# Kernel tuning notes

Hardware: AMD Instinct MI355X
Metric: run time of the kernel (lower is better)

The kernel has to match this reference:

```python
import jax, jax.numpy as jnp
import numpy as np

B, C, N = 16, 256, 1024
D_QK, D_V, BINS = 64, 256, 32
EPS = 1e-5


def setup_inputs() -> dict:
    key = jax.random.key(0)
    ks = jax.random.split(key, 12)

    def xavier(k, shape):
        fan_in, fan_out = shape[1], shape[0]
        lim = (6.0 / (fan_in + fan_out)) ** 0.5
        return jax.random.uniform(k, shape, jnp.float32, -lim, lim)

    return {
        "x": jax.random.normal(ks[0], (B, C, N), jnp.float32),
        "discrete": jax.random.randint(ks[1], (B, N, 3), 0, BINS),
        "xyz": jax.random.uniform(ks[2], (B, N, 3), jnp.float32),
        "q_w": xavier(ks[3], (D_QK, C)),
        "k_w": xavier(ks[4], (D_QK, C)),
        "v_w": xavier(ks[5], (D_V, C)),
        "v_b": jnp.zeros((D_V,), jnp.float32),
        "trans_w": xavier(ks[6], (C, D_V)),
        "trans_b": jnp.zeros((C,), jnp.float32),
        "bn_gamma": jnp.ones((C,), jnp.float32),
        "bn_beta": jnp.zeros((C,), jnp.float32),
        "x_lt": xavier(ks[7], (2 * BINS - 1, D_QK)),
        "y_lt": xavier(ks[8], (2 * BINS - 1, D_QK)),
        "z_lt": xavier(ks[9], (2 * BINS - 1, D_QK)),
    }


def reference(x, discrete, xyz, q_w, k_w, v_w, v_b, trans_w, trans_b,
              bn_gamma, bn_beta, x_lt, y_lt, z_lt):
    # x: [B,C,N], discrete: [B,N,3] int bin coords in [0,BINS)
    n = x.shape[2]
    x_q = jnp.einsum('dc,bcn->bnd', q_w, x)                      # [B,N,d_qk]
    x_k = jnp.einsum('dc,bcn->bdn', k_w, x)                      # [B,d_qk,N]
    x_v = jnp.einsum('dc,bcn->bdn', v_w, x) + v_b[None, :, None]  # [B,d_v,N]

    energy = jnp.einsum('bnd,bdm->bnm', x_q, x_k)                # [B,N,N]

    def rel_term(lt, d):
        # q @ lookup-table then gather along relative bin index (irregular access)
        ql = jnp.einsum('bnd,rd->bnr', x_q, lt)                  # [B,N,2*BINS-1]
        idx = d[:, None, :] - d[:, :, None] + (BINS - 1)          # [B,N,N]
        return jnp.take_along_axis(ql, idx, axis=2)

    dx, dy, dz = discrete[..., 0], discrete[..., 1], discrete[..., 2]
    energy = energy + rel_term(x_lt, dx) + rel_term(y_lt, dy) + rel_term(z_lt, dz)

    energy = energy / (float(n) ** 0.5)                           # scale == 'root'
    attention = jax.nn.softmax(energy, axis=-1)

    x_r = jnp.einsum('bdn,bnm->bdm', x_v, attention)              # [B,d_v,N]

    # offset=True: trans_conv(x - x_r) -> BN (batch stats) -> ReLU -> residual
    h = x - x_r
    t = jnp.einsum('cd,bdn->bcn', trans_w, h) + trans_b[None, :, None]
    mean = t.mean(axis=(0, 2), keepdims=True)
    var = t.var(axis=(0, 2), keepdims=True)
    t = (t - mean) * jax.lax.rsqrt(var + EPS)
    t = t * bn_gamma[None, :, None] + bn_beta[None, :, None]
    x_r = jax.nn.relu(t)
    return x + x_r
```

## Files before the change

### kernel.cpp

```cpp
#include <hip/hip_runtime.h>
#include <math.h>

#define BB 16
#define CC 256
#define NN 1024
#define DQK_ 64
#define DV_ 256
#define NR 192
#define EPS_F 1e-5f

#define OFF_XT  ((size_t)0)
#define OFF_QB  ((size_t)2097152)
#define OFF_KB  ((size_t)2621440)
#define OFF_QL  ((size_t)3145728)
#define OFF_HT  ((size_t)2097152)
#define OFF_VB  ((size_t)6291456)
#define OFF_ATT ((size_t)8388608)
#define OFF_T   ((size_t)8388608)
#define OFF_WQK ((size_t)16777216)
#define OFF_WV  ((size_t)16793600)
#define OFF_WT  ((size_t)16826368)
#define OFF_LTB ((size_t)16859136)
#define OFF_BNS ((size_t)16865280)
#define OFF_BNQ ((size_t)16865536)

typedef __attribute__((ext_vector_type(8))) short short8;
typedef __attribute__((ext_vector_type(4))) float f32x4;

__device__ __forceinline__ unsigned short f2b(float f) {
    unsigned int u = __float_as_uint(f);
    u = u + 0x7fffu + ((u >> 16) & 1u);
    return (unsigned short)(u >> 16);
}
__device__ __forceinline__ float b2f(unsigned short s) {
    return __uint_as_float(((unsigned int)s) << 16);
}

__global__ __launch_bounds__(256) void k_prep(
    const float* __restrict__ qw, const float* __restrict__ kw,
    const float* __restrict__ vw, const float* __restrict__ tw,
    const float* __restrict__ xlt, const float* __restrict__ ylt,
    const float* __restrict__ zlt,
    unsigned short* __restrict__ Wqk, unsigned short* __restrict__ Wv,
    unsigned short* __restrict__ Wt, unsigned short* __restrict__ LTb,
    float* __restrict__ bnS, float* __restrict__ bnQ)
{
    if (blockIdx.x == 160) {
        bnS[threadIdx.x] = 0.f;
        bnQ[threadIdx.x] = 0.f;
        return;
    }
    if (blockIdx.x > 160) {
        const int o2 = (blockIdx.x - 161) * 256 + threadIdx.x;
        const int e = o2 * 4;
        const int r = e >> 6, d = e & 63;
        const int a = r >> 6, q = r & 63;
        ushort4 u;
        if (q < 63) {
            const float* lt = (a == 0) ? xlt : ((a == 1) ? ylt : zlt);
            const float4 v = *(const float4*)(lt + q * 64 + d);
            u.x = f2b(v.x); u.y = f2b(v.y); u.z = f2b(v.z); u.w = f2b(v.w);
        } else {
            u.x = u.y = u.z = u.w = 0;
        }
        *(ushort4*)(LTb + e) = u;
        return;
    }
    const int o = blockIdx.x * 256 + threadIdx.x;
    const float* src; unsigned short* dst;
    if (o < 8192) {
        const int e = o * 4;
        src = (e < 16384) ? (qw + e) : (kw + e - 16384);
        dst = Wqk + e;
    } else if (o < 24576) {
        const int e = (o - 8192) * 4;
        src = vw + e; dst = Wv + e;
    } else {
        const int e = (o - 24576) * 4;
        src = tw + e; dst = Wt + e;
    }
    const float4 v = *(const float4*)src;
    ushort4 u;
    u.x = f2b(v.x); u.y = f2b(v.y); u.z = f2b(v.z); u.w = f2b(v.w);
    *(ushort4*)dst = u;
}

__global__ __launch_bounds__(256) void k_xt(
    const float* __restrict__ x, unsigned short* __restrict__ xT)
{
    __shared__ float tile[64][68];
    const int b = blockIdx.z;
    const int c0 = blockIdx.y * 64;
    const int n0 = blockIdx.x * 64;
    const int tid = threadIdx.x;
    #pragma unroll
    for (int it = 0; it < 4; ++it) {
        const int r = it * 16 + (tid >> 4);
        const int c4 = (tid & 15) * 4;
        *(float4*)&tile[r][c4] =
            *(const float4*)(x + ((size_t)b * CC + c0 + r) * NN + n0 + c4);
    }
    __syncthreads();
    const int n = tid >> 2;
    const int cg2 = (tid & 3) * 16;
    alignas(16) unsigned short buf[16];
    #pragma unroll
    for (int j = 0; j < 16; ++j) buf[j] = f2b(tile[cg2 + j][n]);
    unsigned short* dst = xT + ((size_t)b * NN + n0 + n) * CC + c0 + cg2;
    *(short8*)dst       = *(const short8*)&buf[0];
    *(short8*)(dst + 8) = *(const short8*)&buf[8];
}

__global__ __launch_bounds__(256) void k_projqk(
    const unsigned short* __restrict__ xT, const unsigned short* __restrict__ Wqk,
    unsigned short* __restrict__ Qb, unsigned short* __restrict__ Kb)
{
    const int b = blockIdx.y;
    const int n0 = blockIdx.x * 32;
    const int tid = threadIdx.x;
    const int l = tid & 63, w = tid >> 6;
    const int l15 = l & 15, l4 = l >> 4;
    const int ng = (w >> 1) * 16, wh = (w & 1) * 64;
    const unsigned short* ap = xT + ((size_t)b * NN + n0 + ng + l15) * CC + l4 * 8;
    const unsigned short* bp = Wqk + ((size_t)(wh + l15)) * CC + l4 * 8;
    f32x4 z = {0.f, 0.f, 0.f, 0.f};
    f32x4 acc[4] = {z, z, z, z};
    #pragma unroll 2
    for (int kk = 0; kk < CC; kk += 32) {
        const short8 a = *(const short8*)(ap + kk);
        short8 bf[4];
        #pragma unroll
        for (int j = 0; j < 4; ++j)
            bf[j] = *(const short8*)(bp + (size_t)j * 16 * CC + kk);
        #pragma unroll
        for (int j = 0; j < 4; ++j)
            acc[j] = __builtin_amdgcn_mfma_f32_16x16x32_bf16(a, bf[j], acc[j], 0, 0, 0);
    }
    #pragma unroll
    for (int j = 0; j < 4; ++j)
        #pragma unroll
        for (int r = 0; r < 4; ++r) {
            const int n = n0 + ng + l4 * 4 + r;
            const int ch = wh + j * 16 + l15;
            const unsigned short v = f2b(acc[j][r]);
            if (ch < 64) Qb[((size_t)b * NN + n) * DQK_ + ch] = v;
            else         Kb[((size_t)b * NN + n) * DQK_ + ch - 64] = v;
        }
}

__global__ __launch_bounds__(256) void k_qlm(
    const unsigned short* __restrict__ Qb, const unsigned short* __restrict__ LTb,
    float* __restrict__ QL)
{
    const int b = blockIdx.y;
    const int n0 = blockIdx.x * 64;
    const int tid = threadIdx.x;
    const int l = tid & 63, w = tid >> 6;
    const int l15 = l & 15, l4 = l >> 4;
    const unsigned short* ap = Qb + ((size_t)b * NN + n0 + w * 16 + l15) * DQK_ + l4 * 8;
    const short8 a0 = *(const short8*)ap;
    const short8 a1 = *(const short8*)(ap + 32);
    f32x4 z = {0.f, 0.f, 0.f, 0.f};
    f32x4 acc[12];
    #pragma unroll
    for (int j = 0; j < 12; ++j) acc[j] = z;
    #pragma unroll
    for (int j = 0; j < 12; ++j) {
        const unsigned short* bp = LTb + (size_t)(j * 16 + l15) * DQK_ + l4 * 8;
        const short8 b0 = *(const short8*)bp;
        const short8 b1 = *(const short8*)(bp + 32);
        acc[j] = __builtin_amdgcn_mfma_f32_16x16x32_bf16(a0, b0, acc[j], 0, 0, 0);
        acc[j] = __builtin_amdgcn_mfma_f32_16x16x32_bf16(a1, b1, acc[j], 0, 0, 0);
    }
    float* qrow0 = QL + ((size_t)b * NN + n0 + w * 16 + l4 * 4) * NR;
    #pragma unroll
    for (int rr = 0; rr < 4; ++rr) {
        float* qr = qrow0 + (size_t)rr * NR + l15;
        #pragma unroll
        for (int j = 0; j < 12; ++j) qr[j * 16] = acc[j][rr];
    }
}

__global__ __launch_bounds__(256) void k_projv(
    const unsigned short* __restrict__ Wv, const unsigned short* __restrict__ xT,
    const float* __restrict__ vb, unsigned short* __restrict__ Vb)
{
    const int b = blockIdx.y;
    const int n0 = blockIdx.x * 32;
    const int tid = threadIdx.x;
    const int l = tid & 63, w = tid >> 6;
    const int l15 = l & 15, l4 = l >> 4;
    const unsigned short* ap = Wv + ((size_t)(w * 64 + l15)) * CC + l4 * 8;
    const unsigned short* bp = xT + ((size_t)b * NN + n0 + l15) * CC + l4 * 8;
    f32x4 z = {0.f, 0.f, 0.f, 0.f};
    f32x4 acc[4][2] = {{z, z}, {z, z}, {z, z}, {z, z}};
    #pragma unroll 2
    for (int kk = 0; kk < CC; kk += 32) {
        short8 af[4], bf[2];
        #pragma unroll
        for (int i = 0; i < 4; ++i)
            af[i] = *(const short8*)(ap + (size_t)i * 16 * CC + kk);
        #pragma unroll
        for (int j = 0; j < 2; ++j)
            bf[j] = *(const short8*)(bp + (size_t)j * 16 * CC + kk);
        #pragma unroll
        for (int i = 0; i < 4; ++i)
            #pragma unroll
            for (int j = 0; j < 2; ++j)
                acc[i][j] = __builtin_amdgcn_mfma_f32_16x16x32_bf16(af[i], bf[j], acc[i][j], 0, 0, 0);
    }
    #pragma unroll
    for (int i = 0; i < 4; ++i)
        #pragma unroll
        for (int r = 0; r < 4; ++r) {
            const int dv = w * 64 + i * 16 + l4 * 4 + r;
            const float bias = vb[dv];
            #pragma unroll
            for (int j = 0; j < 2; ++j) {
                const int n = n0 + j * 16 + l15;
                Vb[((size_t)b * DV_ + dv) * NN + n] = f2b(acc[i][j][r] + bias);
            }
        }
}

__global__ __launch_bounds__(512) void k_attn(
    const unsigned short* __restrict__ Qb, const unsigned short* __restrict__ Kb,
    const float* __restrict__ QL, const int* __restrict__ disc,
    unsigned short* __restrict__ att)
{
    __shared__ float QLs[16][193];
    __shared__ int   dmp[1024];
    __shared__ float redS[8][16];
    const int b = blockIdx.y;
    const int q0 = blockIdx.x * 16;
    const int tid = threadIdx.x;
    const int l = tid & 63, w = tid >> 6;
    const int l15 = l & 15, l4 = l >> 4;

    for (int o = tid; o < 16 * NR; o += 512) {
        const int r = o / NR, c = o - r * NR;
        QLs[r][c] = QL[((size_t)b * NN + q0 + r) * NR + c];
    }
    for (int m = tid; m < NN; m += 512) {
        const size_t base = ((size_t)b * NN + m) * 3;
        dmp[m] = disc[base] | (disc[base + 1] << 8) | (disc[base + 2] << 16);
    }
    __syncthreads();

    const int q = q0 + l15;
    const int dn0 = disc[((size_t)b * NN + q) * 3 + 0] - 31;
    const int dn1 = disc[((size_t)b * NN + q) * 3 + 1] - 31;
    const int dn2 = disc[((size_t)b * NN + q) * 3 + 2] - 31;

    const unsigned short* qp = Qb + ((size_t)b * NN + q) * DQK_ + l4 * 8;
    const short8 qf0 = *(const short8*)qp;
    const short8 qf1 = *(const short8*)(qp + 32);

    const unsigned short* kbase = Kb + (size_t)b * NN * DQK_ + l4 * 8;
    const unsigned short* kp0 = kbase + (size_t)(w * 16 + l15) * DQK_;
    short8 kf0 = *(const short8*)kp0;
    short8 kf1 = *(const short8*)(kp0 + 32);

    float s[32];
    float sum = 0.f;
    #pragma unroll
    for (int t = 0; t < 8; ++t) {
        const int tn = (t < 7) ? t + 1 : 7;
        const unsigned short* kpn = kbase + (size_t)(tn * 128 + w * 16 + l15) * DQK_;
        const short8 nf0 = *(const short8*)kpn;
        const short8 nf1 = *(const short8*)(kpn + 32);
        f32x4 acc = {0.f, 0.f, 0.f, 0.f};
        acc = __builtin_amdgcn_mfma_f32_16x16x32_bf16(kf0, qf0, acc, 0, 0, 0);
        acc = __builtin_amdgcn_mfma_f32_16x16x32_bf16(kf1, qf1, acc, 0, 0, 0);
        const int m0 = t * 128 + w * 16 + l4 * 4;
        const int4 pm4 = *(const int4*)&dmp[m0];
        const int* pmp = (const int*)&pm4;
        #pragma unroll
        for (int r = 0; r < 4; ++r) {
            const int pm = pmp[r];
            const int i0 = (pm & 255) - dn0;
            const int i1 = ((pm >> 8) & 255) - dn1;
            const int i2 = (pm >> 16) - dn2;
            const float rel = QLs[l15][i0] + QLs[l15][64 + i1] + QLs[l15][128 + i2];
            const float e = __expf((acc[r] + rel) * 0.03125f);
            s[t * 4 + r] = e;
            sum += e;
        }
        kf0 = nf0; kf1 = nf1;
    }

    sum += __shfl_xor(sum, 16);
    sum += __shfl_xor(sum, 32);
    if (l < 16) redS[w][l] = sum;
    __syncthreads();
    float tot = redS[0][l15];
    #pragma unroll
    for (int ww = 1; ww < 8; ++ww) tot += redS[ww][l15];
    const float inv = 1.0f / tot;

    #pragma unroll
    for (int t = 0; t < 8; ++t)
        #pragma unroll
        for (int r = 0; r < 4; ++r) {
            const int m = t * 128 + w * 16 + l4 * 4 + r;
            att[((size_t)b * NN + m) * NN + q] = f2b(s[t * 4 + r] * inv);
        }
}

__global__ __launch_bounds__(256) void k_pv(
    const unsigned short* __restrict__ att, const unsigned short* __restrict__ Vb,
    const unsigned short* __restrict__ xT, unsigned short* __restrict__ HT)
{
    __shared__ unsigned short As[2][128][72];
    __shared__ unsigned short Bs[2][128][72];
    const int b = blockIdx.z;
    const int d0 = blockIdx.y * 128;
    const int m0 = blockIdx.x * 128;
    const int tid = threadIdx.x;
    const int l = tid & 63, w = tid >> 6;
    const int l15 = l & 15, l4 = l >> 4;
    const int wm = (w & 1) * 64, wd = (w >> 1) * 64;

    const unsigned short* agbase = att + ((size_t)b * NN + m0) * NN;
    const unsigned short* bgbase = Vb + ((size_t)b * DV_ + d0) * NN;

    f32x4 z = {0.f, 0.f, 0.f, 0.f};
    f32x4 acc[4][4];
    #pragma unroll
    for (int i = 0; i < 4; ++i)
        #pragma unroll
        for (int j = 0; j < 4; ++j) acc[i][j] = z;

    short8 pa[4], pb[4];
    #pragma unroll
    for (int it = 0; it < 4; ++it) {
        const int f = it * 256 + tid, r = f >> 3, c = (f & 7) * 8;
        pa[it] = *(const short8*)(agbase + (size_t)r * NN + c);
        pb[it] = *(const short8*)(bgbase + (size_t)r * NN + c);
    }
    #pragma unroll
    for (int it = 0; it < 4; ++it) {
        const int f = it * 256 + tid, r = f >> 3, c = (f & 7) * 8;
        *(short8*)&As[0][r][c] = pa[it];
        *(short8*)&Bs[0][r][c] = pb[it];
    }
    __syncthreads();

    for (int ks = 0; ks < 16; ++ks) {
        const int cur = ks & 1;
        if (ks < 15) {
            const int nk = (ks + 1) * 64;
            #pragma unroll
            for (int it = 0; it < 4; ++it) {
                const int f = it * 256 + tid, r = f >> 3, c = (f & 7) * 8;
                pa[it] = *(const short8*)(agbase + (size_t)r * NN + nk + c);
                pb[it] = *(const short8*)(bgbase + (size_t)r * NN + nk + c);
            }
        }
        #pragma unroll
        for (int ksub = 0; ksub < 2; ++ksub) {
            short8 af[4], bf[4];
            #pragma unroll
            for (int i = 0; i < 4; ++i)
                af[i] = *(const short8*)&As[cur][wm + i * 16 + l15][ksub * 32 + l4 * 8];
            #pragma unroll
            for (int j = 0; j < 4; ++j)
                bf[j] = *(const short8*)&Bs[cur][wd + j * 16 + l15][ksub * 32 + l4 * 8];
            #pragma unroll
            for (int i = 0; i < 4; ++i)
                #pragma unroll
                for (int j = 0; j < 4; ++j)
                    acc[i][j] = __builtin_amdgcn_mfma_f32_16x16x32_bf16(af[i], bf[j], acc[i][j], 0, 0, 0);
        }
        if (ks < 15) {
            #pragma unroll
            for (int it = 0; it < 4; ++it) {
                const int f = it * 256 + tid, r = f >> 3, c = (f & 7) * 8;
                *(short8*)&As[cur ^ 1][r][c] = pa[it];
                *(short8*)&Bs[cur ^ 1][r][c] = pb[it];
            }
        }
        __syncthreads();
    }

    #pragma unroll
    for (int i = 0; i < 4; ++i)
        #pragma unroll
        for (int r = 0; r < 4; ++r) {
            const int m = m0 + wm + i * 16 + l4 * 4 + r;
            const unsigned short* xrow = xT + ((size_t)b * NN + m) * CC;
            unsigned short* hrow = HT + ((size_t)b * NN + m) * CC;
            #pragma unroll
            for (int j = 0; j < 4; ++j) {
                const int dv = d0 + wd + j * 16 + l15;
                hrow[dv] = f2b(b2f(xrow[dv]) - acc[i][j][r]);
            }
        }
}

__global__ __launch_bounds__(256) void k_trans(
    const unsigned short* __restrict__ Wt, const unsigned short* __restrict__ HT,
    const float* __restrict__ tb, unsigned short* __restrict__ T,
    float* __restrict__ bnS, float* __restrict__ bnQ)
{
    __shared__ float sS[128], sQ[128];
    const int b = blockIdx.z;
    const int c0 = blockIdx.y * 128;
    const int n0 = blockIdx.x * 64;
    const int tid = threadIdx.x;
    const int l = tid & 63, w = tid >> 6;
    const int l15 = l & 15, l4 = l >> 4;
    const int wc = (w & 1) * 64, wn = (w >> 1) * 32;
    if (tid < 128) { sS[tid] = 0.f; sQ[tid] = 0.f; }
    __syncthreads();
    const unsigned short* ap = Wt + ((size_t)(c0 + wc + l15)) * CC + l4 * 8;
    const unsigned short* bp = HT + ((size_t)b * NN + n0 + wn + l15) * CC + l4 * 8;
    f32x4 z = {0.f, 0.f, 0.f, 0.f};
    f32x4 acc[4][2] = {{z, z}, {z, z}, {z, z}, {z, z}};
    #pragma unroll 2
    for (int kk = 0; kk < CC; kk += 32) {
        short8 af[4], bf[2];
        #pragma unroll
        for (int i = 0; i < 4; ++i)
            af[i] = *(const short8*)(ap + (size_t)i * 16 * CC + kk);
        #pragma unroll
        for (int j = 0; j < 2; ++j)
            bf[j] = *(const short8*)(bp + (size_t)j * 16 * CC + kk);
        #pragma unroll
        for (int i = 0; i < 4; ++i)
            #pragma unroll
            for (int j = 0; j < 2; ++j)
                acc[i][j] = __builtin_amdgcn_mfma_f32_16x16x32_bf16(af[i], bf[j], acc[i][j], 0, 0, 0);
    }
    #pragma unroll
    for (int i = 0; i < 4; ++i)
        #pragma unroll
        for (int r = 0; r < 4; ++r) {
            const int cl = wc + i * 16 + l4 * 4 + r;
            const int c = c0 + cl;
            const float bias = tb[c];
            float s = 0.f, q = 0.f;
            #pragma unroll
            for (int j = 0; j < 2; ++j) {
                const int n = n0 + wn + j * 16 + l15;
                const float t = acc[i][j][r] + bias;
                T[((size_t)b * CC + c) * NN + n] = f2b(t);
                s += t; q += t * t;
            }
            s += __shfl_xor(s, 1); s += __shfl_xor(s, 2);
            s += __shfl_xor(s, 4); s += __shfl_xor(s, 8);
            q += __shfl_xor(q, 1); q += __shfl_xor(q, 2);
            q += __shfl_xor(q, 4); q += __shfl_xor(q, 8);
            if (l15 == 0) {
                atomicAdd(&sS[cl], s);
                atomicAdd(&sQ[cl], q);
            }
        }
    __syncthreads();
    if (tid < 128) {
        atomicAdd(&bnS[c0 + tid], sS[tid]);
        atomicAdd(&bnQ[c0 + tid], sQ[tid]);
    }
}

__global__ __launch_bounds__(256) void k_out(
    const float* __restrict__ x, const unsigned short* __restrict__ T,
    const float* __restrict__ gamma, const float* __restrict__ beta,
    const float* __restrict__ bnS, const float* __restrict__ bnQ,
    float* __restrict__ out)
{
    const int i8 = blockIdx.x * 256 + threadIdx.x;
    const int c = (i8 >> 7) & 255;
    const float meanv = bnS[c] * (1.0f / 16384.0f);
    const float varv  = bnQ[c] * (1.0f / 16384.0f) - meanv * meanv;
    const float inv   = rsqrtf(varv + EPS_F);
    const float g = gamma[c] * inv;
    const float be = beta[c];
    const short8 t8 = *(const short8*)(T + (size_t)i8 * 8);
    const unsigned short* tp = (const unsigned short*)&t8;
    const float4 xa = *(const float4*)(x + (size_t)i8 * 8);
    const float4 xb = *(const float4*)(x + (size_t)i8 * 8 + 4);
    float4 oa, ob;
    oa.x = xa.x + fmaxf(g * (b2f(tp[0]) - meanv) + be, 0.0f);
    oa.y = xa.y + fmaxf(g * (b2f(tp[1]) - meanv) + be, 0.0f);
    oa.z = xa.z + fmaxf(g * (b2f(tp[2]) - meanv) + be, 0.0f);
    oa.w = xa.w + fmaxf(g * (b2f(tp[3]) - meanv) + be, 0.0f);
    ob.x = xb.x + fmaxf(g * (b2f(tp[4]) - meanv) + be, 0.0f);
    ob.y = xb.y + fmaxf(g * (b2f(tp[5]) - meanv) + be, 0.0f);
    ob.z = xb.z + fmaxf(g * (b2f(tp[6]) - meanv) + be, 0.0f);
    ob.w = xb.w + fmaxf(g * (b2f(tp[7]) - meanv) + be, 0.0f);
    *(float4*)(out + (size_t)i8 * 8)     = oa;
    *(float4*)(out + (size_t)i8 * 8 + 4) = ob;
}

extern "C" void kernel_launch(void* const* d_in, const int* in_sizes, int n_in,
                              void* d_out, int out_size, void* d_ws, size_t ws_size,
                              hipStream_t stream)
{
    const float* x     = (const float*)d_in[0];
    const int*   disc  = (const int*)d_in[1];
    const float* qw    = (const float*)d_in[3];
    const float* kw    = (const float*)d_in[4];
    const float* vw    = (const float*)d_in[5];
    const float* vb    = (const float*)d_in[6];
    const float* tw    = (const float*)d_in[7];
    const float* tb    = (const float*)d_in[8];
    const float* gamma = (const float*)d_in[9];
    const float* beta  = (const float*)d_in[10];
    const float* xlt   = (const float*)d_in[11];
    const float* ylt   = (const float*)d_in[12];
    const float* zlt   = (const float*)d_in[13];
    float* ws  = (float*)d_ws;
    float* out = (float*)d_out;

    unsigned short* xT  = (unsigned short*)(ws + OFF_XT);
    unsigned short* Qb  = (unsigned short*)(ws + OFF_QB);
    unsigned short* Kbf = (unsigned short*)(ws + OFF_KB);
    float*          QL  = ws + OFF_QL;
    unsigned short* HT  = (unsigned short*)(ws + OFF_HT);
    unsigned short* Vb  = (unsigned short*)(ws + OFF_VB);
    unsigned short* ATT = (unsigned short*)(ws + OFF_ATT);
    unsigned short* T   = (unsigned short*)(ws + OFF_T);
    unsigned short* Wqk = (unsigned short*)(ws + OFF_WQK);
    unsigned short* Wv  = (unsigned short*)(ws + OFF_WV);
    unsigned short* Wt  = (unsigned short*)(ws + OFF_WT);
    unsigned short* LTb = (unsigned short*)(ws + OFF_LTB);
    float*          bnS = ws + OFF_BNS;
    float*          bnQ = ws + OFF_BNQ;

    k_prep  <<<dim3(173), 256, 0, stream>>>(qw, kw, vw, tw, xlt, ylt, zlt,
                                            Wqk, Wv, Wt, LTb, bnS, bnQ);
    k_xt    <<<dim3(16, 4, 16), 256, 0, stream>>>(x, xT);
    k_projqk<<<dim3(32, 16), 256, 0, stream>>>(xT, Wqk, Qb, Kbf);
    k_qlm   <<<dim3(16, 16), 256, 0, stream>>>(Qb, LTb, QL);
    k_projv <<<dim3(32, 16), 256, 0, stream>>>(Wv, xT, vb, Vb);
    k_attn  <<<dim3(64, 16), 512, 0, stream>>>(Qb, Kbf, QL, disc, ATT);
    k_pv    <<<dim3(8, 2, 16), 256, 0, stream>>>(ATT, Vb, xT, HT);
    k_trans <<<dim3(16, 2, 16), 256, 0, stream>>>(Wt, HT, tb, T, bnS, bnQ);
    k_out   <<<dim3(2048), 256, 0, stream>>>(x, T, gamma, beta, bnS, bnQ, out);
}
```

Measured before the change: 132.7 us.

## Fuse prep/transpose, QK/V projections, and compute QL inside attention kernel

Merges weight prep and x transpose into one launch, merges the QK and V projection kernels into one grid with a z-split, and removes the separate QL kernel by computing q·lookup-table products per attention block directly into shared memory. This cuts three kernel launches and removes the global round trip of the fp32 QL buffer. In exchange the attention kernel does extra MFMA work before its softmax loop. k_proj still reads xT written by the previous launch, so ordering is preserved.

```diff
diff --git a/kernel.cpp b/kernel.cpp
--- a/kernel.cpp
+++ b/kernel.cpp
@@ -12,7 +12,6 @@
 #define OFF_XT  ((size_t)0)
 #define OFF_QB  ((size_t)2097152)
 #define OFF_KB  ((size_t)2621440)
-#define OFF_QL  ((size_t)3145728)
 #define OFF_HT  ((size_t)2097152)
 #define OFF_VB  ((size_t)6291456)
 #define OFF_ATT ((size_t)8388608)
@@ -36,7 +35,8 @@
     return __uint_as_float(((unsigned int)s) << 16);
 }
 
-__global__ __launch_bounds__(256) void k_prep(
+__global__ __launch_bounds__(256) void k_prepxt(
+    const float* __restrict__ x, unsigned short* __restrict__ xT,
     const float* __restrict__ qw, const float* __restrict__ kw,
     const float* __restrict__ vw, const float* __restrict__ tw,
     const float* __restrict__ xlt, const float* __restrict__ ylt,
@@ -45,13 +45,39 @@
     unsigned short* __restrict__ Wt, unsigned short* __restrict__ LTb,
     float* __restrict__ bnS, float* __restrict__ bnQ)
 {
-    if (blockIdx.x == 160) {
-        bnS[threadIdx.x] = 0.f;
-        bnQ[threadIdx.x] = 0.f;
+    const int tid = threadIdx.x;
+    if (blockIdx.x < 1024) {
+        __shared__ float tile[64][68];
+        const int id = blockIdx.x;
+        const int n0 = (id & 15) * 64;
+        const int c0 = ((id >> 4) & 3) * 64;
+        const int b  = id >> 6;
+        #pragma unroll
+        for (int it = 0; it < 4; ++it) {
+            const int r = it * 16 + (tid >> 4);
+            const int c4 = (tid & 15) * 4;
+            *(float4*)&tile[r][c4] =
+                *(const float4*)(x + ((size_t)b * CC + c0 + r) * NN + n0 + c4);
+        }
+        __syncthreads();
+        const int n = tid >> 2;
+        const int cg2 = (tid & 3) * 16;
+        alignas(16) unsigned short buf[16];
+        #pragma unroll
+        for (int j = 0; j < 16; ++j) buf[j] = f2b(tile[cg2 + j][n]);
+        unsigned short* dst = xT + ((size_t)b * NN + n0 + n) * CC + c0 + cg2;
+        *(short8*)dst       = *(const short8*)&buf[0];
+        *(short8*)(dst + 8) = *(const short8*)&buf[8];
         return;
     }
-    if (blockIdx.x > 160) {
-        const int o2 = (blockIdx.x - 161) * 256 + threadIdx.x;
+    const int pid = blockIdx.x - 1024;
+    if (pid == 160) {
+        bnS[tid] = 0.f;
+        bnQ[tid] = 0.f;
+        return;
+    }
+    if (pid > 160) {
+        const int o2 = (pid - 161) * 256 + tid;
         const int e = o2 * 4;
         const int r = e >> 6, d = e & 63;
         const int a = r >> 6, q = r & 63;
@@ -66,7 +92,7 @@
         *(ushort4*)(LTb + e) = u;
         return;
     }
-    const int o = blockIdx.x * 256 + threadIdx.x;
+    const int o = pid * 256 + tid;
     const float* src; unsigned short* dst;
     if (o < 8192) {
         const int e = o * 4;
@@ -85,147 +111,81 @@
     *(ushort4*)dst = u;
 }
 
-__global__ __launch_bounds__(256) void k_xt(
-    const float* __restrict__ x, unsigned short* __restrict__ xT)
-{
-    __shared__ float tile[64][68];
-    const int b = blockIdx.z;
-    const int c0 = blockIdx.y * 64;
-    const int n0 = blockIdx.x * 64;
-    const int tid = threadIdx.x;
-    #pragma unroll
-    for (int it = 0; it < 4; ++it) {
-        const int r = it * 16 + (tid >> 4);
-        const int c4 = (tid & 15) * 4;
-        *(float4*)&tile[r][c4] =
-            *(const float4*)(x + ((size_t)b * CC + c0 + r) * NN + n0 + c4);
-    }
-    __syncthreads();
-    const int n = tid >> 2;
-    const int cg2 = (tid & 3) * 16;
-    alignas(16) unsigned short buf[16];
-    #pragma unroll
-    for (int j = 0; j < 16; ++j) buf[j] = f2b(tile[cg2 + j][n]);
-    unsigned short* dst = xT + ((size_t)b * NN + n0 + n) * CC + c0 + cg2;
-    *(short8*)dst       = *(const short8*)&buf[0];
-    *(short8*)(dst + 8) = *(const short8*)&buf[8];
-}
-
-__global__ __launch_bounds__(256) void k_projqk(
+__global__ __launch_bounds__(256) void k_proj(
     const unsigned short* __restrict__ xT, const unsigned short* __restrict__ Wqk,
-    unsigned short* __restrict__ Qb, unsigned short* __restrict__ Kb)
+    const unsigned short* __restrict__ Wv, const float* __restrict__ vb,
+    unsigned short* __restrict__ Qb, unsigned short* __restrict__ Kb,
+    unsigned short* __restrict__ Vb)
 {
     const int b = blockIdx.y;
     const int n0 = blockIdx.x * 32;
     const int tid = threadIdx.x;
     const int l = tid & 63, w = tid >> 6;
     const int l15 = l & 15, l4 = l >> 4;
-    const int ng = (w >> 1) * 16, wh = (w & 1) * 64;
-    const unsigned short* ap = xT + ((size_t)b * NN + n0 + ng + l15) * CC + l4 * 8;
-    const unsigned short* bp = Wqk + ((size_t)(wh + l15)) * CC + l4 * 8;
     f32x4 z = {0.f, 0.f, 0.f, 0.f};
-    f32x4 acc[4] = {z, z, z, z};
-    #pragma unroll 2
-    for (int kk = 0; kk < CC; kk += 32) {
-        const short8 a = *(const short8*)(ap + kk);
-        short8 bf[4];
+    if (blockIdx.z == 0) {
+        const int ng = (w >> 1) * 16, wh = (w & 1) * 64;
+        const unsigned short* ap = xT + ((size_t)b * NN + n0 + ng + l15) * CC + l4 * 8;
+        const unsigned short* bp = Wqk + ((size_t)(wh + l15)) * CC + l4 * 8;
+        f32x4 acc[4] = {z, z, z, z};
+        #pragma unroll 2
+        for (int kk = 0; kk < CC; kk += 32) {
+            const short8 a = *(const short8*)(ap + kk);
+            short8 bf[4];
+            #pragma unroll
+            for (int j = 0; j < 4; ++j)
+                bf[j] = *(const short8*)(bp + (size_t)j * 16 * CC + kk);
+            #pragma unroll
+            for (int j = 0; j < 4; ++j)
+                acc[j] = __builtin_amdgcn_mfma_f32_16x16x32_bf16(a, bf[j], acc[j], 0, 0, 0);
+        }
         #pragma unroll
         for (int j = 0; j < 4; ++j)
-            bf[j] = *(const short8*)(bp + (size_t)j * 16 * CC + kk);
-        #pragma unroll
-        for (int j = 0; j < 4; ++j)
-            acc[j] = __builtin_amdgcn_mfma_f32_16x16x32_bf16(a, bf[j], acc[j], 0, 0, 0);
-    }
-    #pragma unroll
-    for (int j = 0; j < 4; ++j)
-        #pragma unroll
-        for (int r = 0; r < 4; ++r) {
-            const int n = n0 + ng + l4 * 4 + r;
-            const int ch = wh + j * 16 + l15;
-            const unsigned short v = f2b(acc[j][r]);
-            if (ch < 64) Qb[((size_t)b * NN + n) * DQK_ + ch] = v;
-            else         Kb[((size_t)b * NN + n) * DQK_ + ch - 64] = v;
-        }
-}
-
-__global__ __launch_bounds__(256) void k_qlm(
-    const unsigned short* __restrict__ Qb, const unsigned short* __restrict__ LTb,
-    float* __restrict__ QL)
-{
-    const int b = blockIdx.y;
-    const int n0 = blockIdx.x * 64;
-    const int tid = threadIdx.x;
-    const int l = tid & 63, w = tid >> 6;
-    const int l15 = l & 15, l4 = l >> 4;
-    const unsigned short* ap = Qb + ((size_t)b * NN + n0 + w * 16 + l15) * DQK_ + l4 * 8;
-    const short8 a0 = *(const short8*)ap;
-    const short8 a1 = *(const short8*)(ap + 32);
-    f32x4 z = {0.f, 0.f, 0.f, 0.f};
-    f32x4 acc[12];
-    #pragma unroll
-    for (int j = 0; j < 12; ++j) acc[j] = z;
-    #pragma unroll
-    for (int j = 0; j < 12; ++j) {
-        const unsigned short* bp = LTb + (size_t)(j * 16 + l15) * DQK_ + l4 * 8;
-        const short8 b0 = *(const short8*)bp;
-        const short8 b1 = *(const short8*)(bp + 32);
-        acc[j] = __builtin_amdgcn_mfma_f32_16x16x32_bf16(a0, b0, acc[j], 0, 0, 0);
-        acc[j] = __builtin_amdgcn_mfma_f32_16x16x32_bf16(a1, b1, acc[j], 0, 0, 0);
-    }
-    float* qrow0 = QL + ((size_t)b * NN + n0 + w * 16 + l4 * 4) * NR;
-    #pragma unroll
-    for (int rr = 0; rr < 4; ++rr) {
-        float* qr = qrow0 + (size_t)rr * NR + l15;
-        #pragma unroll
-        for (int j = 0; j < 12; ++j) qr[j * 16] = acc[j][rr];
-    }
-}
-
-__global__ __launch_bounds__(256) void k_projv(
-    const unsigned short* __restrict__ Wv, const unsigned short* __restrict__ xT,
-    const float* __restrict__ vb, unsigned short* __restrict__ Vb)
-{
-    const int b = blockIdx.y;
-    const int n0 = blockIdx.x * 32;
-    const int tid = threadIdx.x;
-    const int l = tid & 63, w = tid >> 6;
-    const int l15 = l & 15, l4 = l >> 4;
-    const unsigned short* ap = Wv + ((size_t)(w * 64 + l15)) * CC + l4 * 8;
-    const unsigned short* bp = xT + ((size_t)b * NN + n0 + l15) * CC + l4 * 8;
-    f32x4 z = {0.f, 0.f, 0.f, 0.f};
-    f32x4 acc[4][2] = {{z, z}, {z, z}, {z, z}, {z, z}};
-    #pragma unroll 2
-    for (int kk = 0; kk < CC; kk += 32) {
-        short8 af[4], bf[2];
+            #pragma unroll
+            for (int r = 0; r < 4; ++r) {
+                const int n = n0 + ng + l4 * 4 + r;
+                const int ch = wh + j * 16 + l15;
+                const unsigned short v = f2b(acc[j][r]);
+                if (ch < 64) Qb[((size_t)b * NN + n) * DQK_ + ch] = v;
+                else         Kb[((size_t)b * NN + n) * DQK_ + ch - 64] = v;
+            }
+    } else {
+        const unsigned short* ap = Wv + ((size_t)(w * 64 + l15)) * CC + l4 * 8;
+        const unsigned short* bp = xT + ((size_t)b * NN + n0 + l15) * CC + l4 * 8;
+        f32x4 acc[4][2] = {{z, z}, {z, z}, {z, z}, {z, z}};
+        #pragma unroll 2
+        for (int kk = 0; kk < CC; kk += 32) {
+            short8 af[4], bf[2];
+            #pragma unroll
+            for (int i = 0; i < 4; ++i)
+                af[i] = *(const short8*)(ap + (size_t)i * 16 * CC + kk);
+            #pragma unroll
+            for (int j = 0; j < 2; ++j)
+                bf[j] = *(const short8*)(bp + (size_t)j * 16 * CC + kk);
+            #pragma unroll
+            for (int i = 0; i < 4; ++i)
+                #pragma unroll
+                for (int j = 0; j < 2; ++j)
+                    acc[i][j] = __builtin_amdgcn_mfma_f32_16x16x32_bf16(af[i], bf[j], acc[i][j], 0, 0, 0);
+        }
         #pragma unroll
         for (int i = 0; i < 4; ++i)
-            af[i] = *(const short8*)(ap + (size_t)i * 16 * CC + kk);
-        #pragma unroll
-        for (int j = 0; j < 2; ++j)
-            bf[j] = *(const short8*)(bp + (size_t)j * 16 * CC + kk);
-        #pragma unroll
-        for (int i = 0; i < 4; ++i)
-            #pragma unroll
-            for (int j = 0; j < 2; ++j)
-                acc[i][j] = __builtin_amdgcn_mfma_f32_16x16x32_bf16(af[i], bf[j], acc[i][j], 0, 0, 0);
-    }
-    #pragma unroll
-    for (int i = 0; i < 4; ++i)
-        #pragma unroll
-        for (int r = 0; r < 4; ++r) {
-            const int dv = w * 64 + i * 16 + l4 * 4 + r;
-            const float bias = vb[dv];
-            #pragma unroll
-            for (int j = 0; j < 2; ++j) {
-                const int n = n0 + j * 16 + l15;
-                Vb[((size_t)b * DV_ + dv) * NN + n] = f2b(acc[i][j][r] + bias);
-            }
-        }
+            #pragma unroll
+            for (int r = 0; r < 4; ++r) {
+                const int dv = w * 64 + i * 16 + l4 * 4 + r;
+                const float bias = vb[dv];
+                #pragma unroll
+                for (int j = 0; j < 2; ++j) {
+                    const int n = n0 + j * 16 + l15;
+                    Vb[((size_t)b * DV_ + dv) * NN + n] = f2b(acc[i][j][r] + bias);
+                }
+            }
+    }
 }
 
 __global__ __launch_bounds__(512) void k_attn(
     const unsigned short* __restrict__ Qb, const unsigned short* __restrict__ Kb,
-    const float* __restrict__ QL, const int* __restrict__ disc,
+    const unsigned short* __restrict__ LTb, const int* __restrict__ disc,
     unsigned short* __restrict__ att)
 {
     __shared__ float QLs[16][193];
@@ -237,15 +197,10 @@
     const int l = tid & 63, w = tid >> 6;
     const int l15 = l & 15, l4 = l >> 4;
 
-    for (int o = tid; o < 16 * NR; o += 512) {
-        const int r = o / NR, c = o - r * NR;
-        QLs[r][c] = QL[((size_t)b * NN + q0 + r) * NR + c];
-    }
     for (int m = tid; m < NN; m += 512) {
         const size_t base = ((size_t)b * NN + m) * 3;
         dmp[m] = disc[base] | (disc[base + 1] << 8) | (disc[base + 2] << 16);
     }
-    __syncthreads();
 
     const int q = q0 + l15;
     const int dn0 = disc[((size_t)b * NN + q) * 3 + 0] - 31;
@@ -255,6 +210,23 @@
     const unsigned short* qp = Qb + ((size_t)b * NN + q) * DQK_ + l4 * 8;
     const short8 qf0 = *(const short8*)qp;
     const short8 qf1 = *(const short8*)(qp + 32);
+
+    if (w < 6) {
+        #pragma unroll
+        for (int jj = 0; jj < 2; ++jj) {
+            const int j = w * 2 + jj;
+            const unsigned short* bp2 = LTb + (size_t)(j * 16 + l15) * DQK_ + l4 * 8;
+            const short8 b0 = *(const short8*)bp2;
+            const short8 b1 = *(const short8*)(bp2 + 32);
+            f32x4 a2 = {0.f, 0.f, 0.f, 0.f};
+            a2 = __builtin_amdgcn_mfma_f32_16x16x32_bf16(qf0, b0, a2, 0, 0, 0);
+            a2 = __builtin_amdgcn_mfma_f32_16x16x32_bf16(qf1, b1, a2, 0, 0, 0);
+            #pragma unroll
+            for (int rr = 0; rr < 4; ++rr)
+                QLs[l4 * 4 + rr][j * 16 + l15] = a2[rr];
+        }
+    }
+    __syncthreads();
 
     const unsigned short* kbase = Kb + (size_t)b * NN * DQK_ + l4 * 8;
     const unsigned short* kp0 = kbase + (size_t)(w * 16 + l15) * DQK_;
@@ -516,7 +488,6 @@
     unsigned short* xT  = (unsigned short*)(ws + OFF_XT);
     unsigned short* Qb  = (unsigned short*)(ws + OFF_QB);
     unsigned short* Kbf = (unsigned short*)(ws + OFF_KB);
-    float*          QL  = ws + OFF_QL;
     unsigned short* HT  = (unsigned short*)(ws + OFF_HT);
     unsigned short* Vb  = (unsigned short*)(ws + OFF_VB);
     unsigned short* ATT = (unsigned short*)(ws + OFF_ATT);
@@ -528,13 +499,11 @@
     float*          bnS = ws + OFF_BNS;
     float*          bnQ = ws + OFF_BNQ;
 
-    k_prep  <<<dim3(173), 256, 0, stream>>>(qw, kw, vw, tw, xlt, ylt, zlt,
-                                            Wqk, Wv, Wt, LTb, bnS, bnQ);
-    k_xt    <<<dim3(16, 4, 16), 256, 0, stream>>>(x, xT);
-    k_projqk<<<dim3(32, 16), 256, 0, stream>>>(xT, Wqk, Qb, Kbf);
-    k_qlm   <<<dim3(16, 16), 256, 0, stream>>>(Qb, LTb, QL);
-    k_projv <<<dim3(32, 16), 256, 0, stream>>>(Wv, xT, vb, Vb);
-    k_attn  <<<dim3(64, 16), 512, 0, stream>>>(Qb, Kbf, QL, disc, ATT);
+    k_prepxt<<<dim3(1197), 256, 0, stream>>>(x, xT, qw, kw, vw, tw,
+                                             xlt, ylt, zlt,
+                                             Wqk, Wv, Wt, LTb, bnS, bnQ);
+    k_proj  <<<dim3(32, 16, 2), 256, 0, stream>>>(xT, Wqk, Wv, vb, Qb, Kbf, Vb);
+    k_attn  <<<dim3(64, 16), 512, 0, stream>>>(Qb, Kbf, LTb, disc, ATT);
     k_pv    <<<dim3(8, 2, 16), 256, 0, stream>>>(ATT, Vb, xT, HT);
     k_trans <<<dim3(16, 2, 16), 256, 0, stream>>>(Wt, HT, tb, T, bnS, bnQ);
     k_out   <<<dim3(2048), 256, 0, stream>>>(x, T, gamma, beta, bnS, bnQ, out);
```

New measurement: 118.7 us. 10.6% less time.
